# Kernel optimization log

Hardware: AMD Instinct MI355X
Metric: run time of the kernel (lower is better)

## Reference

```python
import jax, jax.numpy as jnp
import numpy as np

CHANNELS = 512
NUM_HEADS = 8


def setup_inputs() -> dict:
    key = jax.random.key(0)
    ks = jax.random.split(key, 5)
    c = CHANNELS
    x = jax.random.normal(ks[0], (8, c, 32, 32), dtype=jnp.float32)
    # nn.Linear(channels, 3*channels) weight is (out, in); keep torch layout
    w_qkv = jax.random.normal(ks[1], (3 * c, c), dtype=jnp.float32) / np.sqrt(c)
    b_qkv = jax.random.normal(ks[2], (3 * c,), dtype=jnp.float32) * 0.01
    w_o = jax.random.normal(ks[3], (c, c), dtype=jnp.float32) / np.sqrt(c)
    b_o = jax.random.normal(ks[4], (c,), dtype=jnp.float32) * 0.01
    return {"x": x, "w_qkv": w_qkv, "b_qkv": b_qkv, "w_o": w_o, "b_o": b_o}


def reference(x, w_qkv, b_qkv, w_o, b_o):
    b, c, h, w = x.shape
    nh = NUM_HEADS
    hd = c // nh
    # b c h w -> b (h w) c
    xs = jnp.transpose(x.reshape(b, c, h * w), (0, 2, 1))  # [b, s, c]
    qkv = xs @ w_qkv.T + b_qkv                              # [b, s, 3c]
    q, k, v = qkv[..., :c], qkv[..., c:2 * c], qkv[..., 2 * c:]
    s = h * w
    q = q.reshape(b, s, nh, hd).transpose(0, 2, 1, 3)       # [b, nh, s, hd]
    k = k.reshape(b, s, nh, hd).transpose(0, 2, 1, 3)
    v = v.reshape(b, s, nh, hd).transpose(0, 2, 1, 3)
    scores = jnp.einsum('bnqd,bnkd->bnqk', q, k) / np.sqrt(hd).astype(np.float32)
    probs = jax.nn.softmax(scores, axis=-1)                 # [b, nh, s, s]
    av = jnp.einsum('bnqk,bnkd->bqnd', probs, v).reshape(b, s, c)
    out = av @ w_o.T + b_o                                  # [b, s, c]
    # b (h w) c -> b c h w
    return jnp.transpose(out, (0, 2, 1)).reshape(b, c, h, w)
```

## Files before the change

### kernel.cpp

```cpp
#include <hip/hip_runtime.h>
#include <cstddef>
#include <cstdint>

#define CH 512
#define SEQ 1024
#define NH 8
#define HD 64

typedef unsigned short u16;
typedef unsigned int u32;
typedef __attribute__((ext_vector_type(8))) short bf16x8;
typedef __attribute__((ext_vector_type(4))) float f32x4;
typedef __attribute__((ext_vector_type(4))) unsigned short u16x4;

#define SCLQ 0.1803368801111204f

__device__ __forceinline__ u16 f2bf(float f) {
  unsigned u = __float_as_uint(f);
  u += 0x7fffu + ((u >> 16) & 1u);
  return (u16)(u >> 16);
}
__device__ __forceinline__ float bf2f(u16 h) {
  return __uint_as_float(((unsigned)h) << 16);
}
__device__ __forceinline__ u32 cvtpk(float lo, float hi) {
  u32 r;
  asm("v_cvt_pk_bf16_f32 %0, %1, %2" : "=v"(r) : "v"(lo), "v"(hi));
  return r;
}

__device__ __forceinline__ void gld16(void* lds, const void* g) {
  __builtin_amdgcn_global_load_lds(
      (const __attribute__((address_space(1))) unsigned int*)g,
      (__attribute__((address_space(3))) unsigned int*)lds, 16, 0, 0);
}

__device__ __forceinline__ f32x4 mfma16(bf16x8 a, bf16x8 b, f32x4 c) {
  return __builtin_amdgcn_mfma_f32_16x16x32_bf16(a, b, c, 0, 0, 0);
}

__global__ __launch_bounds__(256) void split_both(
    const float* __restrict__ wqkv, u16* __restrict__ wqkv_h, u16* __restrict__ wqkv_l,
    const float* __restrict__ wo, u16* __restrict__ wo_h, u16* __restrict__ wo_l)
{
  const int b = blockIdx.x;
  const float* in; u16* hi; u16* lo; int i;
  if (b < 768) { in = wqkv; hi = wqkv_h; lo = wqkv_l; i = b * 256 + threadIdx.x; }
  else         { in = wo;   hi = wo_h;   lo = wo_l;   i = (b - 768) * 256 + threadIdx.x; }
  float4 v = ((const float4*)in)[i];
  u16x4 h, l;
  h[0] = f2bf(v.x); l[0] = f2bf(v.x - bf2f(h[0]));
  h[1] = f2bf(v.y); l[1] = f2bf(v.y - bf2f(h[1]));
  h[2] = f2bf(v.z); l[2] = f2bf(v.z - bf2f(h[2]));
  h[3] = f2bf(v.w); l[3] = f2bf(v.w - bf2f(h[3]));
  ((u16x4*)hi)[i] = h;
  ((u16x4*)lo)[i] = l;
}

__global__ __launch_bounds__(256) void transpose_split(
    const float* __restrict__ x, u16* __restrict__ xh, u16* __restrict__ xl)
{
  __shared__ float tile[64][65];
  const int s0 = blockIdx.x * 64, c0 = blockIdx.y * 64, bz = blockIdx.z;
  const int t = threadIdx.x;
  #pragma unroll
  for (int p = 0; p < 16; ++p) {
    int i = p * 256 + t;
    int cl = i >> 6, sl = i & 63;
    tile[cl][sl] = x[((size_t)bz * CH + c0 + cl) * SEQ + s0 + sl];
  }
  __syncthreads();
  #pragma unroll
  for (int p = 0; p < 16; ++p) {
    int i = p * 256 + t;
    int sl = i >> 6, cl = i & 63;
    float v = tile[cl][sl];
    u16 h = f2bf(v);
    size_t idx = ((size_t)bz * SEQ + s0 + sl) * CH + c0 + cl;
    xh[idx] = h;
    xl[idx] = f2bf(v - bf2f(h));
  }
}

template<int MODE, int BM>
__global__ __launch_bounds__(256, 2) void gemm_hilo(
    const u16* __restrict__ Ah, const u16* __restrict__ Al,
    const u16* __restrict__ BTh, const u16* __restrict__ BTl,
    const float* __restrict__ bias,
    void* __restrict__ o0, void* __restrict__ o1, void* __restrict__ o2,
    void* __restrict__ o3, void* __restrict__ o4)
{
  constexpr int WM = BM / 2;
  constexpr int MI = WM / 16;
  const int bx = blockIdx.x, by = blockIdx.y, bz = blockIdx.z;
  const int m0 = by * BM, n0 = bx * 128;
  const char* Ahc = (const char*)Ah;
  const char* Alc = (const char*)Al;
  const char* Bhc = (const char*)BTh + (size_t)bz * SEQ * CH * 2;
  const char* Blc = (const char*)BTl + (size_t)bz * SEQ * CH * 2;

  __shared__ __align__(16) u16 As[BM * 64];
  __shared__ __align__(16) u16 Bs[128 * 64];

  const int t = threadIdx.x, w = t >> 6, lane = t & 63;
  const int lr = lane & 15, lg = lane >> 4;
  const int wr = w >> 1, wc = w & 1;

  f32x4 acc[MI][4];
  #pragma unroll
  for (int i = 0; i < MI; ++i)
    #pragma unroll
    for (int j = 0; j < 4; ++j) acc[i][j] = (f32x4){0.f, 0.f, 0.f, 0.f};

  for (int k0 = 0; k0 < CH; k0 += 32) {
    __syncthreads();
    #pragma unroll
    for (int p = 0; p < BM / 32; ++p) {
      const int ldsoff = p * 4096 + w * 1024 + lane * 16;
      const int m = ldsoff >> 7;
      const int W = ldsoff & 127;
      const int Wp = W ^ ((m & 7) << 4);
      const char* src = (Wp < 64 ? Ahc : Alc) + ((size_t)(m0 + m) * CH + k0) * 2 + (Wp & 63);
      gld16((char*)As + p * 4096 + w * 1024, src);
    }
    #pragma unroll
    for (int p = 0; p < 4; ++p) {
      const int ldsoff = p * 4096 + w * 1024 + lane * 16;
      const int n = ldsoff >> 7;
      const int W = ldsoff & 127;
      const int Wp = W ^ ((n & 7) << 4);
      const char* src = (Wp < 64 ? Bhc : Blc) + ((size_t)(n0 + n) * CH + k0) * 2 + (Wp & 63);
      gld16((char*)Bs + p * 4096 + w * 1024, src);
    }
    __syncthreads();

    bf16x8 Afh[MI], Afl[MI], Bfh[4], Bfl[4];
    #pragma unroll
    for (int mi = 0; mi < MI; ++mi) {
      const int m = wr * WM + mi * 16 + lr;
      const int swz = (m & 7) << 4;
      Afh[mi] = *(const bf16x8*)((const char*)As + m * 128 + ((lg * 16) ^ swz));
      Afl[mi] = *(const bf16x8*)((const char*)As + m * 128 + ((64 + lg * 16) ^ swz));
    }
    #pragma unroll
    for (int ni = 0; ni < 4; ++ni) {
      const int n = wc * 64 + ni * 16 + lr;
      const int swz = (n & 7) << 4;
      Bfh[ni] = *(const bf16x8*)((const char*)Bs + n * 128 + ((lg * 16) ^ swz));
      Bfl[ni] = *(const bf16x8*)((const char*)Bs + n * 128 + ((64 + lg * 16) ^ swz));
    }
    #pragma unroll
    for (int mi = 0; mi < MI; ++mi) {
      #pragma unroll
      for (int ni = 0; ni < 4; ++ni) {
        acc[mi][ni] = mfma16(Afh[mi], Bfh[ni], acc[mi][ni]);
        acc[mi][ni] = mfma16(Afh[mi], Bfl[ni], acc[mi][ni]);
        acc[mi][ni] = mfma16(Afl[mi], Bfh[ni], acc[mi][ni]);
      }
    }
  }

  if constexpr (MODE == 0) {
    float* Out = (float*)o0 + (size_t)bz * CH * SEQ;
    #pragma unroll
    for (int mi = 0; mi < MI; ++mi) {
      const int mb = m0 + wr * WM + mi * 16 + lg * 4;
      #pragma unroll
      for (int r = 0; r < 4; ++r) {
        const float bv = bias[mb + r];
        #pragma unroll
        for (int ni = 0; ni < 4; ++ni) {
          const int n = n0 + wc * 64 + ni * 16 + lr;
          Out[(size_t)(mb + r) * SEQ + n] = acc[mi][ni][r] + bv;
        }
      }
    }
  } else {
    u16* qh = (u16*)o0; u16* ql = (u16*)o1;
    u16* kh = (u16*)o2;
    u16* vh = (u16*)o4;
    #pragma unroll
    for (int mi = 0; mi < MI; ++mi) {
      const int mb = m0 + wr * WM + mi * 16 + lg * 4;
      const int sec = mb >> 9;
      const int h = (mb >> 6) & 7;
      const int d = mb & 63;
      const size_t bh = (size_t)bz * NH + h;
      const float b0 = bias[mb + 0], b1 = bias[mb + 1], b2 = bias[mb + 2], b3 = bias[mb + 3];
      #pragma unroll
      for (int ni = 0; ni < 4; ++ni) {
        const int n = n0 + wc * 64 + ni * 16 + lr;
        float c0 = acc[mi][ni][0] + b0;
        float c1 = acc[mi][ni][1] + b1;
        float c2 = acc[mi][ni][2] + b2;
        float c3 = acc[mi][ni][3] + b3;
        if (sec == 2) {
          u16* dst = vh + (bh * HD + d) * SEQ + n;
          dst[0 * SEQ] = f2bf(c0);
          dst[1 * SEQ] = f2bf(c1);
          dst[2 * SEQ] = f2bf(c2);
          dst[3 * SEQ] = f2bf(c3);
        } else if (sec == 1) {
          u16* dsth = kh + (bh * SEQ + n) * HD + d;
          u16x4 hv;
          hv[0] = f2bf(c0); hv[1] = f2bf(c1); hv[2] = f2bf(c2); hv[3] = f2bf(c3);
          *(u16x4*)dsth = hv;
        } else {
          c0 *= SCLQ; c1 *= SCLQ; c2 *= SCLQ; c3 *= SCLQ;
          u16* dsth = qh + (bh * SEQ + n) * HD + d;
          u16* dstl = ql + (bh * SEQ + n) * HD + d;
          u16x4 hv, lv;
          hv[0] = f2bf(c0); lv[0] = f2bf(c0 - bf2f(hv[0]));
          hv[1] = f2bf(c1); lv[1] = f2bf(c1 - bf2f(hv[1]));
          hv[2] = f2bf(c2); lv[2] = f2bf(c2 - bf2f(hv[2]));
          hv[3] = f2bf(c3); lv[3] = f2bf(c3 - bf2f(hv[3]));
          *(u16x4*)dsth = hv;
          *(u16x4*)dstl = lv;
        }
      }
    }
  }
}

__global__ __launch_bounds__(256, 4) void attn_mfma(
    const u16* __restrict__ q_h, const u16* __restrict__ q_l,
    const u16* __restrict__ k_h, const u16* __restrict__ v_h,
    u16* __restrict__ av_h, u16* __restrict__ av_l)
{
  const int bid = blockIdx.x;
  const int xcd = bid & 7, rr = bid >> 3;
  const int qt = rr & 15, ghi = rr >> 4;
  const int g = ghi * 8 + xcd;
  const int hh = g & 7, bz = g >> 3;
  const int bhead = bz * NH + hh;
  const int s0 = qt * 64;
  const int t = threadIdx.x, w = t >> 6, lane = t & 63;
  const int lr = lane & 15, lg = lane >> 4;
  const int gsw = ((lr & 7) << 4) | (lr & 8);

  __shared__ __align__(16) char SH[40960];

  bf16x8 QBh[2], QBl[2];
  {
    const size_t qrow = (size_t)bhead * SEQ + s0 + w * 16 + lr;
    #pragma unroll
    for (int ks = 0; ks < 2; ++ks) {
      QBh[ks] = *(const bf16x8*)((const char*)q_h + qrow * 128 + ks * 64 + lg * 16);
      QBl[ks] = *(const bf16x8*)((const char*)q_l + qrow * 128 + ks * 64 + lg * 16);
    }
  }

  const char* Khb = (const char*)k_h + (size_t)bhead * SEQ * 128;
  const char* Vbb = (const char*)v_h + (size_t)bhead * HD * 2048;

  const char* kp[2][4];
  #pragma unroll
  for (int ks = 0; ks < 2; ++ks)
    #pragma unroll
    for (int ni = 0; ni < 4; ++ni) {
      const int row = ni * 16 + lr;
      kp[ks][ni] = SH + row * 128 + ((ks * 64 + lg * 16) ^ ((row & 7) << 4));
    }
  char* pwp = SH + 32768 + w * 2048 + lr * 128;
  char* pw[4];
  #pragma unroll
  for (int ni = 0; ni < 4; ++ni) pw[ni] = pwp + ((ni * 32 + lg * 8) ^ gsw);
  const char* pr[2][2];
  #pragma unroll
  for (int ks = 0; ks < 2; ++ks)
    #pragma unroll
    for (int h2 = 0; h2 < 2; ++h2)
      pr[ks][h2] = pwp + ((ks * 64 + lg * 16 + h2 * 8) ^ gsw);

  auto STAGE = [&](int buf, int tile) {
    const char* ksrc = Khb + (size_t)tile * 8192;
    const char* vsrc = Vbb + (size_t)tile * 128;
    #pragma unroll
    for (int p = 0; p < 2; ++p) {
      const int ldsoff = w * 2048 + p * 1024 + lane * 16;
      const int r = ldsoff >> 7;
      const int Wp = (ldsoff & 127) ^ ((r & 7) << 4);
      gld16(SH + buf * 8192 + ldsoff, ksrc + r * 128 + Wp);
      gld16(SH + 16384 + buf * 8192 + ldsoff, vsrc + (size_t)r * 2048 + Wp);
    }
  };

  union { u32 u[4]; bf16x8 v; } ones;
  ones.u[0] = ones.u[1] = ones.u[2] = ones.u[3] = 0x3f803f80u;

  float mreg = -1e30f;
  f32x4 ls = (f32x4){0.f, 0.f, 0.f, 0.f};
  f32x4 oacc[4];
  #pragma unroll
  for (int ni = 0; ni < 4; ++ni) oacc[ni] = (f32x4){0.f, 0.f, 0.f, 0.f};

  STAGE(0, 0);
  __syncthreads();

  #pragma unroll
  for (int kt = 0; kt < 16; ++kt) {
    const int cur = kt & 1;
    if (kt < 15) STAGE(cur ^ 1, kt + 1);

    f32x4 sc[4];
    #pragma unroll
    for (int ni = 0; ni < 4; ++ni) sc[ni] = (f32x4){0.f, 0.f, 0.f, 0.f};
    #pragma unroll
    for (int ks = 0; ks < 2; ++ks) {
      bf16x8 kf[4];
      #pragma unroll
      for (int ni = 0; ni < 4; ++ni)
        kf[ni] = *(const bf16x8*)(kp[ks][ni] + cur * 8192);
      __builtin_amdgcn_s_setprio(1);
      #pragma unroll
      for (int ni = 0; ni < 4; ++ni) {
        sc[ni] = mfma16(kf[ni], QBh[ks], sc[ni]);
        sc[ni] = mfma16(kf[ni], QBl[ks], sc[ni]);
      }
      __builtin_amdgcn_s_setprio(0);
    }

    float tm = fmaxf(fmaxf(sc[0][0], sc[0][1]), fmaxf(sc[0][2], sc[0][3]));
    #pragma unroll
    for (int ni = 1; ni < 4; ++ni)
      tm = fmaxf(tm, fmaxf(fmaxf(sc[ni][0], sc[ni][1]), fmaxf(sc[ni][2], sc[ni][3])));
    tm = fmaxf(tm, __shfl_xor(tm, 16));
    tm = fmaxf(tm, __shfl_xor(tm, 32));

    if (!__all(tm <= mreg + 8.0f)) {
      const float mn = fmaxf(mreg, tm);
      const float alv = exp2f(mreg - mn);
      mreg = mn;
      float alr[4];
      #pragma unroll
      for (int r = 0; r < 4; ++r) alr[r] = __shfl(alv, lg * 4 + r);
      #pragma unroll
      for (int ni = 0; ni < 4; ++ni)
        #pragma unroll
        for (int r = 0; r < 4; ++r) oacc[ni][r] *= alr[r];
      #pragma unroll
      for (int r = 0; r < 4; ++r) ls[r] *= alr[r];
    }

    #pragma unroll
    for (int ni = 0; ni < 4; ++ni) {
      const float p0 = exp2f(sc[ni][0] - mreg);
      const float p1 = exp2f(sc[ni][1] - mreg);
      const float p2 = exp2f(sc[ni][2] - mreg);
      const float p3 = exp2f(sc[ni][3] - mreg);
      *(uint2*)pw[ni] = make_uint2(cvtpk(p0, p1), cvtpk(p2, p3));
    }

    #pragma unroll
    for (int ks = 0; ks < 2; ++ks) {
      bf16x8 vb[4];
      #pragma unroll
      for (int ni = 0; ni < 4; ++ni)
        vb[ni] = *(const bf16x8*)(kp[ks][ni] + 16384 + cur * 8192);
      const uint2 a = *(const uint2*)pr[ks][0];
      const uint2 b = *(const uint2*)pr[ks][1];
      union { u32 u[4]; bf16x8 v; } pu;
      pu.u[0] = a.x; pu.u[1] = a.y; pu.u[2] = b.x; pu.u[3] = b.y;
      __builtin_amdgcn_s_setprio(1);
      #pragma unroll
      for (int ni = 0; ni < 4; ++ni)
        oacc[ni] = mfma16(pu.v, vb[ni], oacc[ni]);
      ls = mfma16(pu.v, ones.v, ls);
      __builtin_amdgcn_s_setprio(0);
    }

    __syncthreads();
  }

  #pragma unroll
  for (int r = 0; r < 4; ++r) {
    const float invr = 1.f / ls[r];
    const int s = s0 + w * 16 + lg * 4 + r;
    #pragma unroll
    for (int ni = 0; ni < 4; ++ni) {
      const int c = hh * HD + ni * 16 + lr;
      const size_t idx = ((size_t)bz * SEQ + s) * CH + c;
      const float v = oacc[ni][r] * invr;
      const u16 hb = f2bf(v);
      av_h[idx] = hb;
      av_l[idx] = f2bf(v - bf2f(hb));
    }
  }
}

extern "C" void kernel_launch(void* const* d_in, const int* in_sizes, int n_in,
                              void* d_out, int out_size, void* d_ws, size_t ws_size,
                              hipStream_t stream) {
  const float* x     = (const float*)d_in[0];
  const float* w_qkv = (const float*)d_in[1];
  const float* b_qkv = (const float*)d_in[2];
  const float* w_o   = (const float*)d_in[3];
  const float* b_o   = (const float*)d_in[4];
  float* out = (float*)d_out;

  char* ws = (char*)d_ws;
  const size_t SZ = (size_t)8 * SEQ * CH * 2;
  u16* xt_h = (u16*)(ws + 0 * SZ);
  u16* xt_l = (u16*)(ws + 1 * SZ);
  u16* q_h  = (u16*)(ws + 2 * SZ);
  u16* q_l  = (u16*)(ws + 3 * SZ);
  u16* k_h  = (u16*)(ws + 4 * SZ);
  u16* v_h  = (u16*)(ws + 6 * SZ);
  u16* wqkv_h = (u16*)(ws + 7 * SZ);
  u16* wqkv_l = wqkv_h + (size_t)1536 * 512;
  u16* wo_h   = wqkv_l + (size_t)1536 * 512;
  u16* wo_l   = wo_h + (size_t)512 * 512;

  split_both<<<1024, 256, 0, stream>>>(w_qkv, wqkv_h, wqkv_l, w_o, wo_h, wo_l);
  transpose_split<<<dim3(16, 8, 8), 256, 0, stream>>>(x, xt_h, xt_l);

  gemm_hilo<1, 128><<<dim3(8, 12, 8), 256, 0, stream>>>(
      wqkv_h, wqkv_l, xt_h, xt_l, b_qkv,
      (void*)q_h, (void*)q_l, (void*)k_h, nullptr, (void*)v_h);

  attn_mfma<<<dim3(1024), 256, 0, stream>>>(
      q_h, q_l, k_h, v_h, xt_h, xt_l);

  gemm_hilo<0, 64><<<dim3(8, 8, 8), 256, 0, stream>>>(
      wo_h, wo_l, xt_h, xt_l, b_o,
      (void*)out, nullptr, nullptr, nullptr, nullptr);
}
```

Baseline: 182.8 us.

## Keep attention probabilities in registers via permuted K rows; merge prep kernels

The attention kernel no longer writes softmax probabilities to LDS and reads them back in MFMA A-operand layout. Instead, K rows are loaded into LDS in a permuted order so each lane's score outputs already match the operand layout for the PV MFMA, and the packed bf16 values are used straight from registers. This removes the LDS round trip and cuts shared memory from 40KB to 32KB, which may raise occupancy. Separately, the weight split and x transpose/split kernels are fused into one launch to save a kernel launch. The row permutation must exactly match the MFMA lane mapping or results will be wrong.

```diff
diff --git a/kernel.cpp b/kernel.cpp
--- a/kernel.cpp
+++ b/kernel.cpp
@@ -39,46 +39,46 @@
   return __builtin_amdgcn_mfma_f32_16x16x32_bf16(a, b, c, 0, 0, 0);
 }
 
-__global__ __launch_bounds__(256) void split_both(
+__global__ __launch_bounds__(256) void prep(
+    const float* __restrict__ x, u16* __restrict__ xh, u16* __restrict__ xl,
     const float* __restrict__ wqkv, u16* __restrict__ wqkv_h, u16* __restrict__ wqkv_l,
     const float* __restrict__ wo, u16* __restrict__ wo_h, u16* __restrict__ wo_l)
 {
-  const int b = blockIdx.x;
-  const float* in; u16* hi; u16* lo; int i;
-  if (b < 768) { in = wqkv; hi = wqkv_h; lo = wqkv_l; i = b * 256 + threadIdx.x; }
-  else         { in = wo;   hi = wo_h;   lo = wo_l;   i = (b - 768) * 256 + threadIdx.x; }
-  float4 v = ((const float4*)in)[i];
-  u16x4 h, l;
-  h[0] = f2bf(v.x); l[0] = f2bf(v.x - bf2f(h[0]));
-  h[1] = f2bf(v.y); l[1] = f2bf(v.y - bf2f(h[1]));
-  h[2] = f2bf(v.z); l[2] = f2bf(v.z - bf2f(h[2]));
-  h[3] = f2bf(v.w); l[3] = f2bf(v.w - bf2f(h[3]));
-  ((u16x4*)hi)[i] = h;
-  ((u16x4*)lo)[i] = l;
-}
-
-__global__ __launch_bounds__(256) void transpose_split(
-    const float* __restrict__ x, u16* __restrict__ xh, u16* __restrict__ xl)
-{
   __shared__ float tile[64][65];
-  const int s0 = blockIdx.x * 64, c0 = blockIdx.y * 64, bz = blockIdx.z;
+  const int bid = blockIdx.x;
   const int t = threadIdx.x;
-  #pragma unroll
-  for (int p = 0; p < 16; ++p) {
-    int i = p * 256 + t;
-    int cl = i >> 6, sl = i & 63;
-    tile[cl][sl] = x[((size_t)bz * CH + c0 + cl) * SEQ + s0 + sl];
-  }
-  __syncthreads();
-  #pragma unroll
-  for (int p = 0; p < 16; ++p) {
-    int i = p * 256 + t;
-    int sl = i >> 6, cl = i & 63;
-    float v = tile[cl][sl];
-    u16 h = f2bf(v);
-    size_t idx = ((size_t)bz * SEQ + s0 + sl) * CH + c0 + cl;
-    xh[idx] = h;
-    xl[idx] = f2bf(v - bf2f(h));
+  if (bid < 1024) {
+    const int s0 = (bid & 15) * 64, c0 = ((bid >> 4) & 7) * 64, bz = bid >> 7;
+    #pragma unroll
+    for (int p = 0; p < 16; ++p) {
+      int i = p * 256 + t;
+      int cl = i >> 6, sl = i & 63;
+      tile[cl][sl] = x[((size_t)bz * CH + c0 + cl) * SEQ + s0 + sl];
+    }
+    __syncthreads();
+    #pragma unroll
+    for (int p = 0; p < 16; ++p) {
+      int i = p * 256 + t;
+      int sl = i >> 6, cl = i & 63;
+      float v = tile[cl][sl];
+      u16 h = f2bf(v);
+      size_t idx = ((size_t)bz * SEQ + s0 + sl) * CH + c0 + cl;
+      xh[idx] = h;
+      xl[idx] = f2bf(v - bf2f(h));
+    }
+  } else {
+    const int b = bid - 1024;
+    const float* in; u16* hi; u16* lo; int i;
+    if (b < 768) { in = wqkv; hi = wqkv_h; lo = wqkv_l; i = b * 256 + t; }
+    else         { in = wo;   hi = wo_h;   lo = wo_l;   i = (b - 768) * 256 + t; }
+    float4 v = ((const float4*)in)[i];
+    u16x4 h, l;
+    h[0] = f2bf(v.x); l[0] = f2bf(v.x - bf2f(h[0]));
+    h[1] = f2bf(v.y); l[1] = f2bf(v.y - bf2f(h[1]));
+    h[2] = f2bf(v.z); l[2] = f2bf(v.z - bf2f(h[2]));
+    h[3] = f2bf(v.w); l[3] = f2bf(v.w - bf2f(h[3]));
+    ((u16x4*)hi)[i] = h;
+    ((u16x4*)lo)[i] = l;
   }
 }
 
@@ -236,9 +236,8 @@
   const int s0 = qt * 64;
   const int t = threadIdx.x, w = t >> 6, lane = t & 63;
   const int lr = lane & 15, lg = lane >> 4;
-  const int gsw = ((lr & 7) << 4) | (lr & 8);
-
-  __shared__ __align__(16) char SH[40960];
+
+  __shared__ __align__(16) char SH[32768];
 
   bf16x8 QBh[2], QBl[2];
   {
@@ -261,16 +260,6 @@
       const int row = ni * 16 + lr;
       kp[ks][ni] = SH + row * 128 + ((ks * 64 + lg * 16) ^ ((row & 7) << 4));
     }
-  char* pwp = SH + 32768 + w * 2048 + lr * 128;
-  char* pw[4];
-  #pragma unroll
-  for (int ni = 0; ni < 4; ++ni) pw[ni] = pwp + ((ni * 32 + lg * 8) ^ gsw);
-  const char* pr[2][2];
-  #pragma unroll
-  for (int ks = 0; ks < 2; ++ks)
-    #pragma unroll
-    for (int h2 = 0; h2 < 2; ++h2)
-      pr[ks][h2] = pwp + ((ks * 64 + lg * 16 + h2 * 8) ^ gsw);
 
   auto STAGE = [&](int buf, int tile) {
     const char* ksrc = Khb + (size_t)tile * 8192;
@@ -279,8 +268,9 @@
     for (int p = 0; p < 2; ++p) {
       const int ldsoff = w * 2048 + p * 1024 + lane * 16;
       const int r = ldsoff >> 7;
+      const int pr_ = ((r >> 5) << 5) | (((r >> 2) & 3) << 3) | (((r >> 4) & 1) << 2) | (r & 3);
       const int Wp = (ldsoff & 127) ^ ((r & 7) << 4);
-      gld16(SH + buf * 8192 + ldsoff, ksrc + r * 128 + Wp);
+      gld16(SH + buf * 8192 + ldsoff, ksrc + pr_ * 128 + Wp);
       gld16(SH + 16384 + buf * 8192 + ldsoff, vsrc + (size_t)r * 2048 + Wp);
     }
   };
@@ -342,30 +332,31 @@
       for (int r = 0; r < 4; ++r) ls[r] *= alr[r];
     }
 
+    u32 pk0[4], pk1[4];
     #pragma unroll
     for (int ni = 0; ni < 4; ++ni) {
       const float p0 = exp2f(sc[ni][0] - mreg);
       const float p1 = exp2f(sc[ni][1] - mreg);
       const float p2 = exp2f(sc[ni][2] - mreg);
       const float p3 = exp2f(sc[ni][3] - mreg);
-      *(uint2*)pw[ni] = make_uint2(cvtpk(p0, p1), cvtpk(p2, p3));
+      pk0[ni] = cvtpk(p0, p1);
+      pk1[ni] = cvtpk(p2, p3);
     }
 
     #pragma unroll
     for (int ks = 0; ks < 2; ++ks) {
+      union { u32 u[4]; bf16x8 v; } pa;
+      pa.u[0] = pk0[2 * ks];     pa.u[1] = pk1[2 * ks];
+      pa.u[2] = pk0[2 * ks + 1]; pa.u[3] = pk1[2 * ks + 1];
       bf16x8 vb[4];
       #pragma unroll
       for (int ni = 0; ni < 4; ++ni)
         vb[ni] = *(const bf16x8*)(kp[ks][ni] + 16384 + cur * 8192);
-      const uint2 a = *(const uint2*)pr[ks][0];
-      const uint2 b = *(const uint2*)pr[ks][1];
-      union { u32 u[4]; bf16x8 v; } pu;
-      pu.u[0] = a.x; pu.u[1] = a.y; pu.u[2] = b.x; pu.u[3] = b.y;
       __builtin_amdgcn_s_setprio(1);
       #pragma unroll
       for (int ni = 0; ni < 4; ++ni)
-        oacc[ni] = mfma16(pu.v, vb[ni], oacc[ni]);
-      ls = mfma16(pu.v, ones.v, ls);
+        oacc[ni] = mfma16(pa.v, vb[ni], oacc[ni]);
+      ls = mfma16(pa.v, ones.v, ls);
       __builtin_amdgcn_s_setprio(0);
     }
 
@@ -411,8 +402,7 @@
   u16* wo_h   = wqkv_l + (size_t)1536 * 512;
   u16* wo_l   = wo_h + (size_t)512 * 512;
 
-  split_both<<<1024, 256, 0, stream>>>(w_qkv, wqkv_h, wqkv_l, w_o, wo_h, wo_l);
-  transpose_split<<<dim3(16, 8, 8), 256, 0, stream>>>(x, xt_h, xt_l);
+  prep<<<2048, 256, 0, stream>>>(x, xt_h, xt_l, w_qkv, wqkv_h, wqkv_l, w_o, wo_h, wo_l);
 
   gemm_hilo<1, 128><<<dim3(8, 12, 8), 256, 0, stream>>>(
       wqkv_h, wqkv_l, xt_h, xt_l, b_qkv,
```

Result: faster. 175.9 us (-3.8%).
